# Optimization experiments

Measured on AMD Instinct MI355X. Metric: run time of the kernel, lower is better.

## Reference

```python
import jax, jax.numpy as jnp
import numpy as np

NEG_SLOPE = 0.2

def leaky_relu(x):
    return jnp.where(x >= 0, x, NEG_SLOPE * x)

def conv1x1(x, w, b):
    # x: [n,c,h,w], w: [o,c], b: [o]
    return jnp.einsum('nchw,oc->nohw', x, w) + b[None, :, None, None]

def setup_inputs() -> dict:
    key = jax.random.key(0)
    ks = jax.random.split(key, 7)
    n, c, h, w = 4, 64, 80, 80
    scale = 1.0 / np.sqrt(c)
    return {
        'x': jax.random.normal(ks[0], (n, c, h, w), dtype=jnp.float32),
        'w1': jax.random.normal(ks[1], (c, c), dtype=jnp.float32) * scale,
        'b1': jax.random.normal(ks[2], (c,), dtype=jnp.float32) * 0.01,
        'w2': jax.random.normal(ks[3], (c, c), dtype=jnp.float32) * scale,
        'b2': jax.random.normal(ks[4], (c,), dtype=jnp.float32) * 0.01,
        'w3': jax.random.normal(ks[5], (c, c), dtype=jnp.float32) * scale,
        'b3': jax.random.normal(ks[6], (c,), dtype=jnp.float32) * 0.01,
    }

def reference(x, w1, b1, w2, b2, w3, b3):
    n, c, h, w = x.shape
    e1 = leaky_relu(conv1x1(x, w1, b1))  # [n,c,h,w]
    e2 = leaky_relu(conv1x1(x, w2, b2))
    asm = leaky_relu(conv1x1(x, w3, b3))
    # q: [n, hw, c]; k: [n, c, hw]
    q = e1.transpose(0, 2, 3, 1).reshape(n, h * w, c)
    k = e2.reshape(n, c, h * w)
    score = jax.nn.softmax(jnp.matmul(q, k), axis=2)  # [n, hw, hw]
    v = asm.reshape(n, c, h * w).transpose(0, 2, 1)   # [n, hw, c]
    out = jnp.matmul(score, v)                        # [n, hw, c]
    return out.transpose(0, 2, 1).reshape(n, c, h, w)
```

## Files before the change

kernel.cpp:

```cpp
#include <hip/hip_runtime.h>


typedef __attribute__((ext_vector_type(8))) unsigned short us8;
typedef __attribute__((ext_vector_type(4))) unsigned short us4;
typedef __attribute__((ext_vector_type(8))) __bf16 bf16x8;
typedef __attribute__((ext_vector_type(16))) float f32x16;

#define HW 6400
#define L2E 1.44269504088896340736f
#define SHIFT 32.0f
#define KS 4
#define ITERS 25

union V8 { us8 s; us4 h[2]; bf16x8 b; unsigned u4[4]; };

__device__ __forceinline__ unsigned short f32_to_bf16(float f) {
  unsigned u = __float_as_uint(f);
  u += 0x7fffu + ((u >> 16) & 1u);
  return (unsigned short)(u >> 16);
}

__device__ __forceinline__ unsigned pack_bf16x2(float a, float b) {
#if __has_builtin(__builtin_amdgcn_cvt_pk_bf16_f32)
  auto v = __builtin_amdgcn_cvt_pk_bf16_f32(a, b);
  unsigned u;
  __builtin_memcpy(&u, &v, 4);
  return u;
#else
  unsigned ua = __float_as_uint(a); ua += 0x7fffu + ((ua >> 16) & 1u);
  unsigned ub = __float_as_uint(b); ub += 0x7fffu + ((ub >> 16) & 1u);
  return (ua >> 16) | (ub & 0xffff0000u);
#endif
}

__global__ __launch_bounds__(256, 4) void conv_kernel(
    const float* __restrict__ x,
    const float* __restrict__ w1, const float* __restrict__ b1,
    const float* __restrict__ w2, const float* __restrict__ b2,
    const float* __restrict__ w3, const float* __restrict__ b3,
    unsigned short* __restrict__ Qg, unsigned short* __restrict__ Kg,
    unsigned short* __restrict__ Vg) {
  __shared__ __align__(16) float xs[64 * 68];
  const int t = threadIdx.x;
  const int n = blockIdx.y;
  const int p0 = blockIdx.x * 64;
  const int k = blockIdx.z;

  {
    const int c = t >> 2, part = t & 3;
    const float* src = x + ((size_t)(n * 64 + c) * HW + p0 + part * 16);
    float* dst = xs + c * 68 + part * 16;
#pragma unroll
    for (int i = 0; i < 4; ++i)
      *(float4*)(dst + i * 4) = *(const float4*)(src + i * 4);
  }

  const float* wm = (k == 0) ? w1 : (k == 1) ? w2 : w3;
  const float* bm = (k == 0) ? b1 : (k == 1) ? b2 : b3;
  const int p = t & 63;
  const int cg = __builtin_amdgcn_readfirstlane(t >> 6);

  __syncthreads();

  float acc[16];
#pragma unroll
  for (int i = 0; i < 16; ++i) acc[i] = bm[cg * 16 + i];
#pragma unroll 1
  for (int c4 = 0; c4 < 16; ++c4) {
    float4 wv[16];
#pragma unroll
    for (int i = 0; i < 16; ++i)
      wv[i] = *(const float4*)(wm + (cg * 16 + i) * 64 + c4 * 4);
    const float xv0 = xs[(c4 * 4 + 0) * 68 + p];
    const float xv1 = xs[(c4 * 4 + 1) * 68 + p];
    const float xv2 = xs[(c4 * 4 + 2) * 68 + p];
    const float xv3 = xs[(c4 * 4 + 3) * 68 + p];
#pragma unroll
    for (int i = 0; i < 16; ++i) {
      acc[i] = fmaf(wv[i].x, xv0, acc[i]);
      acc[i] = fmaf(wv[i].y, xv1, acc[i]);
      acc[i] = fmaf(wv[i].z, xv2, acc[i]);
      acc[i] = fmaf(wv[i].w, xv3, acc[i]);
    }
  }
#pragma unroll
  for (int i = 0; i < 16; ++i)
    acc[i] = fmaxf(acc[i], 0.f) + 0.2f * fminf(acc[i], 0.f);

  if (k == 0) {
    unsigned short u[16];
#pragma unroll
    for (int i = 0; i < 16; ++i) u[i] = f32_to_bf16(acc[i] * L2E);
    unsigned short* dst = Qg + (size_t)(n * HW + p0 + p) * 64 + cg * 16;
    us8 a, b;
#pragma unroll
    for (int j = 0; j < 8; ++j) { a[j] = u[j]; b[j] = u[8 + j]; }
    *(us8*)dst = a;
    *(us8*)(dst + 8) = b;
  } else if (k == 1) {
    unsigned short u[16];
#pragma unroll
    for (int i = 0; i < 16; ++i) u[i] = f32_to_bf16(acc[i]);
    unsigned short* dst = Kg + (size_t)(n * HW + p0 + p) * 64 + cg * 16;
    us8 a, b;
#pragma unroll
    for (int j = 0; j < 8; ++j) { a[j] = u[j]; b[j] = u[8 + j]; }
    *(us8*)dst = a;
    *(us8*)(dst + 8) = b;
  } else {
#pragma unroll
    for (int i = 0; i < 16; ++i)
      Vg[(size_t)(n * 64 + cg * 16 + i) * HW + p0 + p] = f32_to_bf16(acc[i]);
  }
}

__global__ __launch_bounds__(256, 4) void attn_kernel(
    const unsigned short* __restrict__ Qg, const unsigned short* __restrict__ Kg,
    const unsigned short* __restrict__ Vg, float* __restrict__ Opart,
    float* __restrict__ Lpart) {
  __shared__ __align__(16) char smem[36864];
  float* Ot = (float*)smem;

  const int t = threadIdx.x;
  const int w = t >> 6;
  const int lane = t & 63;
  const int l31 = lane & 31;
  const int lh = lane >> 5;
  const int nb = blockIdx.y;
  const int qb = blockIdx.x * 128;
  const int ks = blockIdx.z;
  const int key0 = ks * (HW / KS);

  const unsigned short* qrow =
      Qg + (size_t)(nb * HW + qb + w * 32 + l31) * 64 + lh * 8;
  V8 aQ[4];
#pragma unroll
  for (int kst = 0; kst < 4; ++kst) aQ[kst].s = *(const us8*)(qrow + kst * 16);

  f32x16 accO0, accO1;
#pragma unroll
  for (int r = 0; r < 16; ++r) { accO0[r] = 0.f; accO1[r] = 0.f; }
  float lpart = 0.f;

  const int soff = (t >> 2) * 72 + (t & 3) * 16;
  const unsigned short* ksrc =
      Kg + (size_t)nb * HW * 64 + (size_t)(key0 + (t >> 2)) * 64 + (t & 3) * 16;
  const unsigned short* vsrc =
      Vg + (size_t)nb * 64 * HW + (size_t)(t >> 2) * HW + key0 + (t & 3) * 16;

  V8 kr0, kr1, vr0, vr1;
  kr0.s = *(const us8*)ksrc;
  kr1.s = *(const us8*)(ksrc + 8);
  vr0.s = *(const us8*)vsrc;
  vr1.s = *(const us8*)(vsrc + 8);
  {
    unsigned short* kd = (unsigned short*)smem + soff;
    unsigned short* vd = (unsigned short*)(smem + 18432) + soff;
    *(us8*)kd = kr0.s; *(us8*)(kd + 8) = kr1.s;
    *(us8*)vd = vr0.s; *(us8*)(vd + 8) = vr1.s;
  }
  __syncthreads();

#pragma unroll 1
  for (int jt = 0; jt < ITERS; ++jt) {
    const int b = jt & 1;
    const unsigned short* Kc = (const unsigned short*)(smem + b * 9216);
    const unsigned short* Vc = (const unsigned short*)(smem + 18432 + b * 9216);
    const bool more = (jt + 1 < ITERS);

    if (more) {
      kr0.s = *(const us8*)(ksrc + (jt + 1) * 4096);
      kr1.s = *(const us8*)(ksrc + (jt + 1) * 4096 + 8);
      vr0.s = *(const us8*)(vsrc + (jt + 1) * 64);
      vr1.s = *(const us8*)(vsrc + (jt + 1) * 64 + 8);
    }

    uint2 pkq[2][4];
#pragma unroll
    for (int ni = 0; ni < 2; ++ni) {
      f32x16 sacc;
#pragma unroll
      for (int r = 0; r < 16; ++r) sacc[r] = 0.f;
#pragma unroll
      for (int kst = 0; kst < 4; ++kst) {
        V8 ak;
        ak.s = *(const us8*)(Kc + (ni * 32 + l31) * 72 + kst * 16 + lh * 8);
        sacc = __builtin_amdgcn_mfma_f32_32x32x16_bf16(ak.b, aQ[kst].b, sacc,
                                                       0, 0, 0);
      }
#pragma unroll
      for (int g = 0; g < 4; ++g) {
        const float p0 = __builtin_amdgcn_exp2f(sacc[4 * g + 0] - SHIFT);
        const float p1 = __builtin_amdgcn_exp2f(sacc[4 * g + 1] - SHIFT);
        const float p2 = __builtin_amdgcn_exp2f(sacc[4 * g + 2] - SHIFT);
        const float p3 = __builtin_amdgcn_exp2f(sacc[4 * g + 3] - SHIFT);
        lpart += (p0 + p1) + (p2 + p3);
        pkq[ni][g].x = pack_bf16x2(p0, p1);
        pkq[ni][g].y = pack_bf16x2(p2, p3);
      }
    }

#pragma unroll
    for (int kst = 0; kst < 4; ++kst) {
      const int ni = kst >> 1;
      const int gb = 2 * (kst & 1);
      const uint2 qa = pkq[ni][gb];
      const uint2 qb2 = pkq[ni][gb + 1];
      uint2 send;
      send.x = lh ? qa.x : qb2.x;
      send.y = lh ? qa.y : qb2.y;
      uint2 recv;
      recv.x = __shfl_xor(send.x, 32);
      recv.y = __shfl_xor(send.y, 32);
      const uint2 keep = {lh ? qb2.x : qa.x, lh ? qb2.y : qa.y};
      V8 ap;
      ap.u4[0] = lh ? recv.x : keep.x;
      ap.u4[1] = lh ? recv.y : keep.y;
      ap.u4[2] = lh ? keep.x : recv.x;
      ap.u4[3] = lh ? keep.y : recv.y;
      V8 bv0, bv1;
      bv0.s = *(const us8*)(Vc + l31 * 72 + kst * 16 + lh * 8);
      bv1.s = *(const us8*)(Vc + (32 + l31) * 72 + kst * 16 + lh * 8);
      accO0 = __builtin_amdgcn_mfma_f32_32x32x16_bf16(ap.b, bv0.b, accO0, 0, 0, 0);
      accO1 = __builtin_amdgcn_mfma_f32_32x32x16_bf16(ap.b, bv1.b, accO1, 0, 0, 0);
    }

    if (more) {
      unsigned short* kd = (unsigned short*)(smem + (1 - b) * 9216) + soff;
      unsigned short* vd = (unsigned short*)(smem + 18432 + (1 - b) * 9216) + soff;
      *(us8*)kd = kr0.s; *(us8*)(kd + 8) = kr1.s;
      *(us8*)vd = vr0.s; *(us8*)(vd + 8) = vr1.s;
      __syncthreads();
    }
  }

  const float lsum = lpart + __shfl_xor(lpart, 32);
  if (lh == 0)
    Lpart[((size_t)ks * 4 + nb) * HW + qb + w * 32 + l31] = lsum;

  __syncthreads();
#pragma unroll
  for (int r = 0; r < 16; ++r) {
    const int m = w * 32 + 8 * (r >> 2) + 4 * lh + (r & 3);
    Ot[l31 * 132 + m] = accO0[r];
    Ot[(32 + l31) * 132 + m] = accO1[r];
  }
  __syncthreads();
  {
    const int ch = t >> 2, part = t & 3;
    const float* src = Ot + ch * 132 + part * 32;
    float* dst = Opart + ((size_t)ks * 4 + nb) * (64 * HW) + (size_t)ch * HW +
                 qb + part * 32;
#pragma unroll
    for (int i = 0; i < 8; ++i)
      *(float4*)(dst + i * 4) = *(const float4*)(src + i * 4);
  }
}

__global__ __launch_bounds__(256) void combine_kernel(
    const float* __restrict__ Opart, const float* __restrict__ Lpart,
    float* __restrict__ out) {
  const int tid = blockIdx.x * 256 + threadIdx.x;
  const size_t e = (size_t)tid * 4;
  float4 o = {0.f, 0.f, 0.f, 0.f};
#pragma unroll
  for (int ks = 0; ks < KS; ++ks) {
    const float4 v = *(const float4*)(Opart + (size_t)ks * (4 * 64 * HW) + e);
    o.x += v.x; o.y += v.y; o.z += v.z; o.w += v.w;
  }
  const int n = (int)(e / (64 * HW));
  const int p = (int)(e % HW);
  float4 l = {0.f, 0.f, 0.f, 0.f};
#pragma unroll
  for (int ks = 0; ks < KS; ++ks) {
    const float4 v = *(const float4*)(Lpart + ((size_t)ks * 4 + n) * HW + p);
    l.x += v.x; l.y += v.y; l.z += v.z; l.w += v.w;
  }
  float4 r;
  r.x = o.x / l.x; r.y = o.y / l.y; r.z = o.z / l.z; r.w = o.w / l.w;
  *(float4*)(out + e) = r;
}

extern "C" void kernel_launch(void* const* d_in, const int* in_sizes, int n_in,
                              void* d_out, int out_size, void* d_ws, size_t ws_size,
                              hipStream_t stream) {
  const float* x = (const float*)d_in[0];
  const float* w1 = (const float*)d_in[1];
  const float* b1 = (const float*)d_in[2];
  const float* w2 = (const float*)d_in[3];
  const float* b2 = (const float*)d_in[4];
  const float* w3 = (const float*)d_in[5];
  const float* b3 = (const float*)d_in[6];
  float* out = (float*)d_out;

  unsigned short* Q = (unsigned short*)d_ws;
  unsigned short* K = Q + (size_t)4 * HW * 64;
  unsigned short* V = K + (size_t)4 * HW * 64;
  float* Opart = (float*)(V + (size_t)4 * HW * 64);
  float* Lpart = Opart + (size_t)KS * 4 * 64 * HW;

  conv_kernel<<<dim3(100, 4, 3), 256, 0, stream>>>(x, w1, b1, w2, b2, w3, b3,
                                                   Q, K, V);
  attn_kernel<<<dim3(50, 4, KS), 256, 0, stream>>>(Q, K, V, Opart, Lpart);
  combine_kernel<<<1600, 256, 0, stream>>>(Opart, Lpart, out);
}
```

Baseline: 167.7 us.

## Move conv to split-bf16 MFMA and enlarge attention query tile per wave

The 1x1 conv now runs on MFMA, using a hi/lo bf16 split of weights and inputs (three MFMAs per step) to keep near-fp32 accuracy. One block computes all three projections from a single x tile, and Q/K are written through an LDS transpose. The attention kernel doubles the query rows per wave (64) so each K/V LDS fragment is reused twice, and the key split changes from 4 to 5 chunks. This trades more registers and lower occupancy (launch bounds 2) for fewer LDS reads and faster conv compute, and grid sizes change to match.

```diff
diff --git a/kernel.cpp b/kernel.cpp
--- a/kernel.cpp
+++ b/kernel.cpp
@@ -9,8 +9,8 @@
 #define HW 6400
 #define L2E 1.44269504088896340736f
 #define SHIFT 32.0f
-#define KS 4
-#define ITERS 25
+#define KS 5
+#define ITERS 20
 
 union V8 { us8 s; us4 h[2]; bf16x8 b; unsigned u4[4]; };
 
@@ -19,7 +19,9 @@
   u += 0x7fffu + ((u >> 16) & 1u);
   return (unsigned short)(u >> 16);
 }
-
+__device__ __forceinline__ float bf16_bits_to_f32(unsigned short u) {
+  return __uint_as_float(((unsigned)u) << 16);
+}
 __device__ __forceinline__ unsigned pack_bf16x2(float a, float b) {
 #if __has_builtin(__builtin_amdgcn_cvt_pk_bf16_f32)
   auto v = __builtin_amdgcn_cvt_pk_bf16_f32(a, b);
@@ -33,88 +35,133 @@
 #endif
 }
 
-__global__ __launch_bounds__(256, 4) void conv_kernel(
+__device__ __forceinline__ void split_hilo(const float* f, V8& hi, V8& lo) {
+#pragma unroll
+  for (int j = 0; j < 8; ++j) {
+    const unsigned short h = f32_to_bf16(f[j]);
+    const float r = f[j] - bf16_bits_to_f32(h);
+    hi.s[j] = h;
+    lo.s[j] = f32_to_bf16(r);
+  }
+}
+
+__global__ __launch_bounds__(256, 2) void conv_kernel(
     const float* __restrict__ x,
     const float* __restrict__ w1, const float* __restrict__ b1,
     const float* __restrict__ w2, const float* __restrict__ b2,
     const float* __restrict__ w3, const float* __restrict__ b3,
     unsigned short* __restrict__ Qg, unsigned short* __restrict__ Kg,
     unsigned short* __restrict__ Vg) {
-  __shared__ __align__(16) float xs[64 * 68];
+  __shared__ __align__(16) float xs[64 * 132];
+  __shared__ __align__(16) unsigned short tb[128 * 72];
+
   const int t = threadIdx.x;
   const int n = blockIdx.y;
-  const int p0 = blockIdx.x * 64;
-  const int k = blockIdx.z;
+  const int p0 = blockIdx.x * 128;
+  const int wv = t >> 6;
+  const int lane = t & 63;
+  const int l31 = lane & 31;
+  const int lh = lane >> 5;
+  const int ob = (wv & 1) * 32;
+  const int pw = (wv >> 1) * 64;
 
   {
-    const int c = t >> 2, part = t & 3;
-    const float* src = x + ((size_t)(n * 64 + c) * HW + p0 + part * 16);
-    float* dst = xs + c * 68 + part * 16;
-#pragma unroll
-    for (int i = 0; i < 4; ++i)
+    const int c = t >> 2, qq = t & 3;
+    const float* src = x + ((size_t)(n * 64 + c) * HW + p0 + qq * 32);
+    float* dst = xs + c * 132 + qq * 32;
+#pragma unroll
+    for (int i = 0; i < 8; ++i)
       *(float4*)(dst + i * 4) = *(const float4*)(src + i * 4);
   }
-
-  const float* wm = (k == 0) ? w1 : (k == 1) ? w2 : w3;
-  const float* bm = (k == 0) ? b1 : (k == 1) ? b2 : b3;
-  const int p = t & 63;
-  const int cg = __builtin_amdgcn_readfirstlane(t >> 6);
-
   __syncthreads();
 
-  float acc[16];
-#pragma unroll
-  for (int i = 0; i < 16; ++i) acc[i] = bm[cg * 16 + i];
+  const float* wms[3] = {w1, w2, w3};
+  const float* bms[3] = {b1, b2, b3};
+
 #pragma unroll 1
-  for (int c4 = 0; c4 < 16; ++c4) {
-    float4 wv[16];
-#pragma unroll
-    for (int i = 0; i < 16; ++i)
-      wv[i] = *(const float4*)(wm + (cg * 16 + i) * 64 + c4 * 4);
-    const float xv0 = xs[(c4 * 4 + 0) * 68 + p];
-    const float xv1 = xs[(c4 * 4 + 1) * 68 + p];
-    const float xv2 = xs[(c4 * 4 + 2) * 68 + p];
-    const float xv3 = xs[(c4 * 4 + 3) * 68 + p];
-#pragma unroll
-    for (int i = 0; i < 16; ++i) {
-      acc[i] = fmaf(wv[i].x, xv0, acc[i]);
-      acc[i] = fmaf(wv[i].y, xv1, acc[i]);
-      acc[i] = fmaf(wv[i].z, xv2, acc[i]);
-      acc[i] = fmaf(wv[i].w, xv3, acc[i]);
-    }
-  }
-#pragma unroll
-  for (int i = 0; i < 16; ++i)
-    acc[i] = fmaxf(acc[i], 0.f) + 0.2f * fminf(acc[i], 0.f);
-
-  if (k == 0) {
-    unsigned short u[16];
-#pragma unroll
-    for (int i = 0; i < 16; ++i) u[i] = f32_to_bf16(acc[i] * L2E);
-    unsigned short* dst = Qg + (size_t)(n * HW + p0 + p) * 64 + cg * 16;
-    us8 a, b;
-#pragma unroll
-    for (int j = 0; j < 8; ++j) { a[j] = u[j]; b[j] = u[8 + j]; }
-    *(us8*)dst = a;
-    *(us8*)(dst + 8) = b;
-  } else if (k == 1) {
-    unsigned short u[16];
-#pragma unroll
-    for (int i = 0; i < 16; ++i) u[i] = f32_to_bf16(acc[i]);
-    unsigned short* dst = Kg + (size_t)(n * HW + p0 + p) * 64 + cg * 16;
-    us8 a, b;
-#pragma unroll
-    for (int j = 0; j < 8; ++j) { a[j] = u[j]; b[j] = u[8 + j]; }
-    *(us8*)dst = a;
-    *(us8*)(dst + 8) = b;
-  } else {
-#pragma unroll
-    for (int i = 0; i < 16; ++i)
-      Vg[(size_t)(n * 64 + cg * 16 + i) * HW + p0 + p] = f32_to_bf16(acc[i]);
-  }
-}
-
-__global__ __launch_bounds__(256, 4) void attn_kernel(
+  for (int k = 0; k < 3; ++k) {
+    const float* wm = wms[k];
+    const float* bm = bms[k];
+
+    V8 ah[4], al[4];
+#pragma unroll
+    for (int kst = 0; kst < 4; ++kst) {
+      const float* wr = wm + (size_t)(ob + l31) * 64 + kst * 16 + lh * 8;
+      float wf[8];
+      *(float4*)(wf) = *(const float4*)wr;
+      *(float4*)(wf + 4) = *(const float4*)(wr + 4);
+      split_hilo(wf, ah[kst], al[kst]);
+    }
+
+    f32x16 acc[2];
+#pragma unroll
+    for (int pb = 0; pb < 2; ++pb)
+#pragma unroll
+      for (int r = 0; r < 16; ++r) acc[pb][r] = 0.f;
+
+#pragma unroll
+    for (int kst = 0; kst < 4; ++kst) {
+#pragma unroll
+      for (int pb = 0; pb < 2; ++pb) {
+        float xf[8];
+        const float* xp = xs + (kst * 16 + lh * 8) * 132 + pw + pb * 32 + l31;
+#pragma unroll
+        for (int j = 0; j < 8; ++j) xf[j] = xp[j * 132];
+        V8 bh, bl;
+        split_hilo(xf, bh, bl);
+        acc[pb] = __builtin_amdgcn_mfma_f32_32x32x16_bf16(al[kst].b, bh.b, acc[pb], 0, 0, 0);
+        acc[pb] = __builtin_amdgcn_mfma_f32_32x32x16_bf16(ah[kst].b, bl.b, acc[pb], 0, 0, 0);
+        acc[pb] = __builtin_amdgcn_mfma_f32_32x32x16_bf16(ah[kst].b, bh.b, acc[pb], 0, 0, 0);
+      }
+    }
+
+    if (k < 2) {
+#pragma unroll
+      for (int pb = 0; pb < 2; ++pb) {
+#pragma unroll
+        for (int rq = 0; rq < 4; ++rq) {
+          const int o = ob + 8 * rq + 4 * lh;
+          const int pcol = pw + pb * 32 + l31;
+          float v[4];
+#pragma unroll
+          for (int j = 0; j < 4; ++j) {
+            float a = acc[pb][4 * rq + j] + bm[o + j];
+            a = fmaxf(a, 0.f) + 0.2f * fminf(a, 0.f);
+            if (k == 0) a *= L2E;
+            v[j] = a;
+          }
+          unsigned* dst = (unsigned*)(tb + pcol * 72 + o);
+          dst[0] = pack_bf16x2(v[0], v[1]);
+          dst[1] = pack_bf16x2(v[2], v[3]);
+        }
+      }
+      __syncthreads();
+      {
+        const int p = t >> 1, half = t & 1;
+        const unsigned short* src = tb + p * 72 + half * 32;
+        unsigned short* dst = (k == 0 ? Qg : Kg) +
+                              (size_t)(n * HW + p0 + p) * 64 + half * 32;
+#pragma unroll
+        for (int i = 0; i < 4; ++i) *(us8*)(dst + i * 8) = *(const us8*)(src + i * 8);
+      }
+      __syncthreads();
+    } else {
+#pragma unroll
+      for (int pb = 0; pb < 2; ++pb) {
+#pragma unroll
+        for (int r = 0; r < 16; ++r) {
+          const int o = ob + 8 * (r >> 2) + 4 * lh + (r & 3);
+          const int pcol = pw + pb * 32 + l31;
+          float a = acc[pb][r] + bm[o];
+          a = fmaxf(a, 0.f) + 0.2f * fminf(a, 0.f);
+          Vg[(size_t)(n * 64 + o) * HW + p0 + pcol] = f32_to_bf16(a);
+        }
+      }
+    }
+  }
+}
+
+__global__ __launch_bounds__(256, 2) void attn_kernel(
     const unsigned short* __restrict__ Qg, const unsigned short* __restrict__ Kg,
     const unsigned short* __restrict__ Vg, float* __restrict__ Opart,
     float* __restrict__ Lpart) {
@@ -127,20 +174,27 @@
   const int l31 = lane & 31;
   const int lh = lane >> 5;
   const int nb = blockIdx.y;
-  const int qb = blockIdx.x * 128;
+  const int qb = blockIdx.x * 256;
   const int ks = blockIdx.z;
   const int key0 = ks * (HW / KS);
 
-  const unsigned short* qrow =
-      Qg + (size_t)(nb * HW + qb + w * 32 + l31) * 64 + lh * 8;
-  V8 aQ[4];
-#pragma unroll
-  for (int kst = 0; kst < 4; ++kst) aQ[kst].s = *(const us8*)(qrow + kst * 16);
-
-  f32x16 accO0, accO1;
-#pragma unroll
-  for (int r = 0; r < 16; ++r) { accO0[r] = 0.f; accO1[r] = 0.f; }
-  float lpart = 0.f;
+  V8 aQ[2][4];
+#pragma unroll
+  for (int qh = 0; qh < 2; ++qh) {
+    const unsigned short* qrow =
+        Qg + (size_t)(nb * HW + qb + w * 64 + qh * 32 + l31) * 64 + lh * 8;
+#pragma unroll
+    for (int kst = 0; kst < 4; ++kst) aQ[qh][kst].s = *(const us8*)(qrow + kst * 16);
+  }
+
+  f32x16 accO[2][2];
+#pragma unroll
+  for (int qh = 0; qh < 2; ++qh)
+#pragma unroll
+    for (int ci = 0; ci < 2; ++ci)
+#pragma unroll
+      for (int r = 0; r < 16; ++r) accO[qh][ci][r] = 0.f;
+  float lp[2] = {0.f, 0.f};
 
   const int soff = (t >> 2) * 72 + (t & 3) * 16;
   const unsigned short* ksrc =
@@ -175,54 +229,70 @@
       vr1.s = *(const us8*)(vsrc + (jt + 1) * 64 + 8);
     }
 
-    uint2 pkq[2][4];
-#pragma unroll
-    for (int ni = 0; ni < 2; ++ni) {
-      f32x16 sacc;
-#pragma unroll
-      for (int r = 0; r < 16; ++r) sacc[r] = 0.f;
+    V8 ak[2][4];
+#pragma unroll
+    for (int ni = 0; ni < 2; ++ni)
+#pragma unroll
+      for (int kst = 0; kst < 4; ++kst)
+        ak[ni][kst].s = *(const us8*)(Kc + (ni * 32 + l31) * 72 + kst * 16 + lh * 8);
+
+    uint2 pkq[2][2][4];
+#pragma unroll
+    for (int qh = 0; qh < 2; ++qh) {
+#pragma unroll
+      for (int ni = 0; ni < 2; ++ni) {
+        f32x16 sacc;
+#pragma unroll
+        for (int r = 0; r < 16; ++r) sacc[r] = 0.f;
+#pragma unroll
+        for (int kst = 0; kst < 4; ++kst)
+          sacc = __builtin_amdgcn_mfma_f32_32x32x16_bf16(ak[ni][kst].b,
+                                                         aQ[qh][kst].b, sacc, 0, 0, 0);
+#pragma unroll
+        for (int g = 0; g < 4; ++g) {
+          const float p0 = __builtin_amdgcn_exp2f(sacc[4 * g + 0] - SHIFT);
+          const float p1 = __builtin_amdgcn_exp2f(sacc[4 * g + 1] - SHIFT);
+          const float p2 = __builtin_amdgcn_exp2f(sacc[4 * g + 2] - SHIFT);
+          const float p3 = __builtin_amdgcn_exp2f(sacc[4 * g + 3] - SHIFT);
+          lp[qh] += (p0 + p1) + (p2 + p3);
+          pkq[qh][ni][g].x = pack_bf16x2(p0, p1);
+          pkq[qh][ni][g].y = pack_bf16x2(p2, p3);
+        }
+      }
+    }
+
+    V8 bv[2][4];
+#pragma unroll
+    for (int ci = 0; ci < 2; ++ci)
+#pragma unroll
+      for (int kst = 0; kst < 4; ++kst)
+        bv[ci][kst].s = *(const us8*)(Vc + (ci * 32 + l31) * 72 + kst * 16 + lh * 8);
+
+#pragma unroll
+    for (int qh = 0; qh < 2; ++qh) {
 #pragma unroll
       for (int kst = 0; kst < 4; ++kst) {
-        V8 ak;
-        ak.s = *(const us8*)(Kc + (ni * 32 + l31) * 72 + kst * 16 + lh * 8);
-        sacc = __builtin_amdgcn_mfma_f32_32x32x16_bf16(ak.b, aQ[kst].b, sacc,
-                                                       0, 0, 0);
-      }
-#pragma unroll
-      for (int g = 0; g < 4; ++g) {
-        const float p0 = __builtin_amdgcn_exp2f(sacc[4 * g + 0] - SHIFT);
-        const float p1 = __builtin_amdgcn_exp2f(sacc[4 * g + 1] - SHIFT);
-        const float p2 = __builtin_amdgcn_exp2f(sacc[4 * g + 2] - SHIFT);
-        const float p3 = __builtin_amdgcn_exp2f(sacc[4 * g + 3] - SHIFT);
-        lpart += (p0 + p1) + (p2 + p3);
-        pkq[ni][g].x = pack_bf16x2(p0, p1);
-        pkq[ni][g].y = pack_bf16x2(p2, p3);
-      }
-    }
-
-#pragma unroll
-    for (int kst = 0; kst < 4; ++kst) {
-      const int ni = kst >> 1;
-      const int gb = 2 * (kst & 1);
-      const uint2 qa = pkq[ni][gb];
-      const uint2 qb2 = pkq[ni][gb + 1];
-      uint2 send;
-      send.x = lh ? qa.x : qb2.x;
-      send.y = lh ? qa.y : qb2.y;
-      uint2 recv;
-      recv.x = __shfl_xor(send.x, 32);
-      recv.y = __shfl_xor(send.y, 32);
-      const uint2 keep = {lh ? qb2.x : qa.x, lh ? qb2.y : qa.y};
-      V8 ap;
-      ap.u4[0] = lh ? recv.x : keep.x;
-      ap.u4[1] = lh ? recv.y : keep.y;
-      ap.u4[2] = lh ? keep.x : recv.x;
-      ap.u4[3] = lh ? keep.y : recv.y;
-      V8 bv0, bv1;
-      bv0.s = *(const us8*)(Vc + l31 * 72 + kst * 16 + lh * 8);
-      bv1.s = *(const us8*)(Vc + (32 + l31) * 72 + kst * 16 + lh * 8);
-      accO0 = __builtin_amdgcn_mfma_f32_32x32x16_bf16(ap.b, bv0.b, accO0, 0, 0, 0);
-      accO1 = __builtin_amdgcn_mfma_f32_32x32x16_bf16(ap.b, bv1.b, accO1, 0, 0, 0);
+        const int ni = kst >> 1;
+        const int gb = 2 * (kst & 1);
+        const uint2 qa = pkq[qh][ni][gb];
+        const uint2 qb2 = pkq[qh][ni][gb + 1];
+        uint2 send;
+        send.x = lh ? qa.x : qb2.x;
+        send.y = lh ? qa.y : qb2.y;
+        uint2 recv;
+        recv.x = __shfl_xor(send.x, 32);
+        recv.y = __shfl_xor(send.y, 32);
+        const uint2 keep = {lh ? qb2.x : qa.x, lh ? qb2.y : qa.y};
+        V8 ap;
+        ap.u4[0] = lh ? recv.x : keep.x;
+        ap.u4[1] = lh ? recv.y : keep.y;
+        ap.u4[2] = lh ? keep.x : recv.x;
+        ap.u4[3] = lh ? keep.y : recv.y;
+        accO[qh][0] = __builtin_amdgcn_mfma_f32_32x32x16_bf16(ap.b, bv[0][kst].b,
+                                                              accO[qh][0], 0, 0, 0);
+        accO[qh][1] = __builtin_amdgcn_mfma_f32_32x32x16_bf16(ap.b, bv[1][kst].b,
+                                                              accO[qh][1], 0, 0, 0);
+      }
     }
 
     if (more) {
@@ -234,26 +304,37 @@
     }
   }
 
-  const float lsum = lpart + __shfl_xor(lpart, 32);
-  if (lh == 0)
-    Lpart[((size_t)ks * 4 + nb) * HW + qb + w * 32 + l31] = lsum;
-
-  __syncthreads();
-#pragma unroll
-  for (int r = 0; r < 16; ++r) {
-    const int m = w * 32 + 8 * (r >> 2) + 4 * lh + (r & 3);
-    Ot[l31 * 132 + m] = accO0[r];
-    Ot[(32 + l31) * 132 + m] = accO1[r];
-  }
-  __syncthreads();
-  {
-    const int ch = t >> 2, part = t & 3;
-    const float* src = Ot + ch * 132 + part * 32;
-    float* dst = Opart + ((size_t)ks * 4 + nb) * (64 * HW) + (size_t)ch * HW +
-                 qb + part * 32;
-#pragma unroll
-    for (int i = 0; i < 8; ++i)
-      *(float4*)(dst + i * 4) = *(const float4*)(src + i * 4);
+#pragma unroll
+  for (int qh = 0; qh < 2; ++qh) {
+    const float lsum = lp[qh] + __shfl_xor(lp[qh], 32);
+    if (lh == 0)
+      Lpart[((size_t)ks * 4 + nb) * HW + qb + w * 64 + qh * 32 + l31] = lsum;
+  }
+
+#pragma unroll 1
+  for (int pi = 0; pi < 2; ++pi) {
+    __syncthreads();
+    if ((w >> 1) == pi) {
+#pragma unroll
+      for (int qh = 0; qh < 2; ++qh)
+#pragma unroll
+        for (int ci = 0; ci < 2; ++ci)
+#pragma unroll
+          for (int r = 0; r < 16; ++r) {
+            const int qcol = (w & 1) * 64 + qh * 32 + 8 * (r >> 2) + 4 * lh + (r & 3);
+            Ot[(ci * 32 + l31) * 132 + qcol] = accO[qh][ci][r];
+          }
+    }
+    __syncthreads();
+    {
+      const int ch = t >> 2, part = t & 3;
+      const float* src = Ot + ch * 132 + part * 32;
+      float* dst = Opart + ((size_t)ks * 4 + nb) * (64 * HW) + (size_t)ch * HW +
+                   qb + pi * 128 + part * 32;
+#pragma unroll
+      for (int i = 0; i < 8; ++i)
+        *(float4*)(dst + i * 4) = *(const float4*)(src + i * 4);
+    }
   }
 }
 
@@ -299,8 +380,8 @@
   float* Opart = (float*)(V + (size_t)4 * HW * 64);
   float* Lpart = Opart + (size_t)KS * 4 * 64 * HW;
 
-  conv_kernel<<<dim3(100, 4, 3), 256, 0, stream>>>(x, w1, b1, w2, b2, w3, b3,
-                                                   Q, K, V);
-  attn_kernel<<<dim3(50, 4, KS), 256, 0, stream>>>(Q, K, V, Opart, Lpart);
+  conv_kernel<<<dim3(50, 4), 256, 0, stream>>>(x, w1, b1, w2, b2, w3, b3,
+                                               Q, K, V);
+  attn_kernel<<<dim3(25, 4, KS), 256, 0, stream>>>(Q, K, V, Opart, Lpart);
   combine_kernel<<<1600, 256, 0, stream>>>(Opart, Lpart, out);
 }
```

Result: faster. 154.3 us (-8.0%).
